# Kernel optimization log

Measured on AMD Instinct MI355X. Metric: run time of the kernel, lower is better.

## Reference

```python
import jax, jax.numpy as jnp
import numpy as np

B, T, D = 4, 2048, 2048
H = 16
HO = D // H  # head_out = 128


def setup_inputs() -> dict:
    key = jax.random.key(0)
    ks = jax.random.split(key, 6)
    x = jax.random.normal(ks[0], (B, T, D), dtype=jnp.float32)
    scale = 0.02
    Wq = jax.random.normal(ks[1], (D, D), dtype=jnp.float32) * scale
    Wk = jax.random.normal(ks[2], (D, D), dtype=jnp.float32) * scale
    Wv = jax.random.normal(ks[3], (D, D), dtype=jnp.float32) * scale
    Wp = jax.random.normal(ks[4], (D, D), dtype=jnp.float32) * scale
    bp = jnp.zeros((D,), dtype=jnp.float32)
    return {"x": x, "Wq": Wq, "Wk": Wk, "Wv": Wv, "Wp": Wp, "bp": bp}


def reference(x, Wq, Wk, Wv, Wp, bp):
    b, t, _ = x.shape
    # QKV projections (weights stored [d_in, d_out])
    q = x @ Wq
    k = x @ Wk
    v = x @ Wv
    split = lambda a: a.reshape(b, t, H, HO).transpose(0, 2, 1, 3)  # [b,H,T,ho]
    qh, kh, vh = split(q), split(k), split(v)
    # Feature attention: contract over tokens -> [b,H,ho,ho]
    scores = jnp.einsum('bhtf,bhtg->bhfg', qh, kh) / jnp.sqrt(jnp.float32(HO))
    weights = jax.nn.softmax(scores, axis=-1)  # dropout p=0.0 (identity)
    # feature_alibi: [1/T, 1/(T-1), ..., 1], broadcast over batch/head/feature
    feat_alibi = (1.0 / jnp.arange(t, 0, -1, dtype=jnp.float32)).reshape(1, 1, t, 1)
    vh = vh + feat_alibi
    # (weights @ v^T)^T : ctx[b,h,t,f] = sum_g weights[b,h,f,g] * v[b,h,t,g]
    ctx = jnp.einsum('bhfg,bhtg->bhtf', weights, vh)
    ctx = ctx.transpose(0, 2, 1, 3).reshape(b, t, H * HO)  # [b,T,d_out]
    return ctx @ Wp + bp
```

## Files before the change

### kernel.cpp

```cpp
#include <hip/hip_runtime.h>
#include <hip/hip_bf16.h>


#define Tt 2048
#define Dd 2048
#define Mm 8192

typedef __attribute__((ext_vector_type(4))) float f32x4;
typedef __attribute__((ext_vector_type(8))) short s16x8;
static_assert(sizeof(s16x8) == 16, "frag size");

typedef const __attribute__((address_space(1))) void* gptr_t;
typedef __attribute__((address_space(3))) void* lptr_t;

__device__ __forceinline__ float bf2f(ushort u) {
    union { unsigned int i; float f; } c; c.i = ((unsigned int)u) << 16; return c.f;
}
__device__ __forceinline__ ushort f2bf(float f) {
    union { float f; unsigned int i; } c; c.f = f;
    return (ushort)((c.i + 0x7FFFu + ((c.i >> 16) & 1u)) >> 16);
}
__device__ __forceinline__ void gload16(const void* g, void* l) {
    __builtin_amdgcn_global_load_lds((gptr_t)g, (lptr_t)l, 16, 0, 0);
}
__device__ __forceinline__ s16x8 ldfrag(const char* p) { return *(const s16x8*)p; }

#define MFMA_BF16(d, a, b) \
    d = __builtin_amdgcn_mfma_f32_16x16x32_bf16((a), (b), (d), 0, 0, 0)


__global__ __launch_bounds__(256) void convxT_kernel(const float* __restrict__ x,
        ushort* __restrict__ xb, ushort* __restrict__ xT) {
    __shared__ float tile[64][65];
    const int b = blockIdx.z;
    const int t0 = blockIdx.y * 64, d0 = blockIdx.x * 64;
    const int r4 = threadIdx.x >> 6, c = threadIdx.x & 63;
#pragma unroll
    for (int i = 0; i < 16; i++) {
        const int row = i * 4 + r4;
        const size_t g = ((size_t)b * Tt + t0 + row) * Dd + d0 + c;
        const float val = x[g];
        xb[g] = f2bf(val);
        tile[row][c] = val;
    }
    __syncthreads();
#pragma unroll
    for (int i = 0; i < 16; i++) {
        const int row = i * 4 + r4;
        xT[(size_t)b * ((size_t)Dd * Tt) + (size_t)(d0 + row) * Tt + t0 + c] =
            f2bf(tile[c][row]);
    }
}

__global__ __launch_bounds__(256) void transw_kernel(const float* __restrict__ W0,
        const float* __restrict__ W1, const float* __restrict__ W2,
        const float* __restrict__ W3, ushort* __restrict__ Wt) {
    __shared__ float tile[64][65];
    const int z = blockIdx.z;
    const float* W = (z == 0) ? W0 : (z == 1) ? W1 : (z == 2) ? W2 : W3;
    ushort* dst = Wt + (size_t)z * ((size_t)Dd * Dd);
    const int n0 = blockIdx.x * 64, k0 = blockIdx.y * 64;
    const int r4 = threadIdx.x >> 6, c = threadIdx.x & 63;
#pragma unroll
    for (int i = 0; i < 16; i++) {
        const int row = i * 4 + r4;
        tile[row][c] = W[(size_t)(k0 + row) * Dd + n0 + c];
    }
    __syncthreads();
#pragma unroll
    for (int i = 0; i < 16; i++) {
        const int row = i * 4 + r4;
        dst[(size_t)(n0 + row) * Dd + k0 + c] = f2bf(tile[c][row]);
    }
}


__device__ __forceinline__ void stage_half(char* ldsRegion, const ushort* gRegion,
                                           int ld, int half, int tid) {
#pragma unroll
    for (int j = 0; j < 2; j++) {
        const int Pb = half * 16384 + j * 8192 + (tid >> 6) * 1024;
        const int P = Pb + (tid & 63) * 16;
        const int row = P >> 7;
        const int colb = (P ^ ((row & 7) << 4)) & 127;
        gload16(gRegion + (size_t)row * ld + (colb >> 1), ldsRegion + Pb);
    }
}

template <int MODE>
__global__ __launch_bounds__(512, 2) void gemm256_kernel(
        const ushort* __restrict__ A, const ushort* __restrict__ Bt,
        void* __restrict__ Cv, const float* __restrict__ bias,
        int Kdim, int lda, int ldb, int ldc,
        size_t astride, size_t bstride, size_t cstride) {
    extern __shared__ char lds[];

    const int tid = threadIdx.x;
    const int lane = tid & 63;
    const int w = tid >> 6;
    const int wr = w >> 2, wc = w & 3;
    const int fr = lane & 15, fq = lane >> 4;

    const int bid = blockIdx.x;
    const int cpx = (int)gridDim.x >> 3;
    const int wg = (bid & 7) * cpx + (bid >> 3);
    const int m0 = (wg >> 3) * 256;
    const int n0 = (wg & 7) * 256;

    const ushort* Ag = A + (size_t)blockIdx.z * astride + (size_t)m0 * lda;
    const ushort* Bg = Bt + (size_t)blockIdx.z * bstride + (size_t)n0 * ldb;
    const int NT = Kdim >> 6;

    const int aoff = wr * 16384 + fr * 128;
    const int boff = wc * 8192 + fr * 128;
    const int xo = (fr & 7) << 4;
    const int cp0 = (fq * 16) ^ xo;
    const int cp1 = (64 + fq * 16) ^ xo;

    char* buf0 = lds;
    char* buf1 = lds + 65536;
    const char* Ab0 = buf0 + aoff;
    const char* Bb0 = buf0 + 32768 + boff;
    const char* Ab1 = buf1 + aoff;
    const char* Bb1 = buf1 + 32768 + boff;

    f32x4 acc[8][4];
#pragma unroll
    for (int i = 0; i < 8; i++)
#pragma unroll
        for (int j = 0; j < 4; j++) acc[i][j] = {0.f, 0.f, 0.f, 0.f};

    s16x8 afX[4][2], afY[4][2], bf01[2][2], bf23[2][2];

    {
        stage_half(buf0,         Ag, lda, 0, tid);
        stage_half(buf0,         Ag, lda, 1, tid);
        stage_half(buf0 + 32768, Bg, ldb, 0, tid);
        stage_half(buf0 + 32768, Bg, ldb, 1, tid);
        stage_half(buf1,         Ag + 64, lda, 0, tid);
        stage_half(buf1,         Ag + 64, lda, 1, tid);
        stage_half(buf1 + 32768, Bg + 64, ldb, 0, tid);
        stage_half(buf1 + 32768, Bg + 64, ldb, 1, tid);
        __builtin_amdgcn_sched_barrier(0);
        asm volatile("s_waitcnt vmcnt(8)" ::: "memory");
        __builtin_amdgcn_s_barrier();
    }

    const int NI = NT >> 1;
    for (int j = 0; j < NI; ++j) {
        const int e = 2 * j;
        const bool sAo = (j > 0);
        const bool sE2 = (e + 2 < NT);
        const bool sO2 = (e + 3 < NT);
        const ushort* AgO  = Ag + (size_t)(e + 1) * 64;
        const ushort* AgE2 = Ag + (size_t)(e + 2) * 64;
        const ushort* BgE2 = Bg + (size_t)(e + 2) * 64;
        const ushort* BgO2 = Bg + (size_t)(e + 3) * 64;

#pragma unroll
        for (int m = 0; m < 4; m++) {
            afX[m][0] = ldfrag(Ab0 + m * 2048 + cp0);
            afX[m][1] = ldfrag(Ab0 + m * 2048 + cp1);
        }
#pragma unroll
        for (int n = 0; n < 2; n++) {
            bf01[n][0] = ldfrag(Bb0 + n * 2048 + cp0);
            bf01[n][1] = ldfrag(Bb0 + n * 2048 + cp1);
        }
        if (sAo) stage_half(buf1, AgO, lda, 0, tid);
        __builtin_amdgcn_sched_barrier(0);
        asm volatile("s_waitcnt lgkmcnt(8)" ::: "memory");
        __builtin_amdgcn_s_barrier();
        asm volatile("s_waitcnt lgkmcnt(0)" ::: "memory");
        __builtin_amdgcn_sched_barrier(0);
        __builtin_amdgcn_s_setprio(1);
#pragma unroll
        for (int k = 0; k < 2; k++)
#pragma unroll
            for (int m = 0; m < 4; m++)
#pragma unroll
                for (int n = 0; n < 2; n++) MFMA_BF16(acc[m][n], afX[m][k], bf01[n][k]);
        __builtin_amdgcn_s_setprio(0);
        __builtin_amdgcn_s_barrier();

#pragma unroll
        for (int n = 0; n < 2; n++) {
            bf23[n][0] = ldfrag(Bb0 + (n + 2) * 2048 + cp0);
            bf23[n][1] = ldfrag(Bb0 + (n + 2) * 2048 + cp1);
        }
        if (sAo) stage_half(buf1, AgO, lda, 1, tid);
        __builtin_amdgcn_sched_barrier(0);
        __builtin_amdgcn_s_barrier();
        asm volatile("s_waitcnt lgkmcnt(0)" ::: "memory");
        __builtin_amdgcn_sched_barrier(0);
        __builtin_amdgcn_s_setprio(1);
#pragma unroll
        for (int k = 0; k < 2; k++)
#pragma unroll
            for (int m = 0; m < 4; m++)
#pragma unroll
                for (int n = 0; n < 2; n++) MFMA_BF16(acc[m][n + 2], afX[m][k], bf23[n][k]);
        __builtin_amdgcn_s_setprio(0);
        __builtin_amdgcn_s_barrier();

#pragma unroll
        for (int m = 0; m < 4; m++) {
            afY[m][0] = ldfrag(Ab0 + (m + 4) * 2048 + cp0);
            afY[m][1] = ldfrag(Ab0 + (m + 4) * 2048 + cp1);
        }
        if (sE2) stage_half(buf0 + 32768, BgE2, ldb, 0, tid);
        __builtin_amdgcn_sched_barrier(0);
        __builtin_amdgcn_s_barrier();
        asm volatile("s_waitcnt lgkmcnt(0)" ::: "memory");
        __builtin_amdgcn_sched_barrier(0);
        __builtin_amdgcn_s_setprio(1);
#pragma unroll
        for (int k = 0; k < 2; k++)
#pragma unroll
            for (int m = 0; m < 4; m++)
#pragma unroll
                for (int n = 0; n < 2; n++) MFMA_BF16(acc[m + 4][n], afY[m][k], bf01[n][k]);
        __builtin_amdgcn_s_setprio(0);
        __builtin_amdgcn_s_barrier();

        if (sE2) stage_half(buf0 + 32768, BgE2, ldb, 1, tid);
        __builtin_amdgcn_sched_barrier(0);
        __builtin_amdgcn_s_setprio(1);
#pragma unroll
        for (int k = 0; k < 2; k++)
#pragma unroll
            for (int m = 0; m < 4; m++)
#pragma unroll
                for (int n = 0; n < 2; n++) MFMA_BF16(acc[m + 4][n + 2], afY[m][k], bf23[n][k]);
        __builtin_amdgcn_s_setprio(0);
        __builtin_amdgcn_sched_barrier(0);
        if (sE2) asm volatile("s_waitcnt vmcnt(4)" ::: "memory");
        else     asm volatile("s_waitcnt vmcnt(0)" ::: "memory");
        __builtin_amdgcn_s_barrier();

#pragma unroll
        for (int m = 0; m < 4; m++) {
            afX[m][0] = ldfrag(Ab1 + m * 2048 + cp0);
            afX[m][1] = ldfrag(Ab1 + m * 2048 + cp1);
        }
#pragma unroll
        for (int n = 0; n < 2; n++) {
            bf01[n][0] = ldfrag(Bb1 + n * 2048 + cp0);
            bf01[n][1] = ldfrag(Bb1 + n * 2048 + cp1);
        }
        if (sE2) stage_half(buf0, AgE2, lda, 0, tid);
        __builtin_amdgcn_sched_barrier(0);
        asm volatile("s_waitcnt lgkmcnt(8)" ::: "memory");
        __builtin_amdgcn_s_barrier();
        asm volatile("s_waitcnt lgkmcnt(0)" ::: "memory");
        __builtin_amdgcn_sched_barrier(0);
        __builtin_amdgcn_s_setprio(1);
#pragma unroll
        for (int k = 0; k < 2; k++)
#pragma unroll
            for (int m = 0; m < 4; m++)
#pragma unroll
                for (int n = 0; n < 2; n++) MFMA_BF16(acc[m][n], afX[m][k], bf01[n][k]);
        __builtin_amdgcn_s_setprio(0);
        __builtin_amdgcn_s_barrier();

#pragma unroll
        for (int n = 0; n < 2; n++) {
            bf23[n][0] = ldfrag(Bb1 + (n + 2) * 2048 + cp0);
            bf23[n][1] = ldfrag(Bb1 + (n + 2) * 2048 + cp1);
        }
        if (sE2) stage_half(buf0, AgE2, lda, 1, tid);
        __builtin_amdgcn_sched_barrier(0);
        __builtin_amdgcn_s_barrier();
        asm volatile("s_waitcnt lgkmcnt(0)" ::: "memory");
        __builtin_amdgcn_sched_barrier(0);
        __builtin_amdgcn_s_setprio(1);
#pragma unroll
        for (int k = 0; k < 2; k++)
#pragma unroll
            for (int m = 0; m < 4; m++)
#pragma unroll
                for (int n = 0; n < 2; n++) MFMA_BF16(acc[m][n + 2], afX[m][k], bf23[n][k]);
        __builtin_amdgcn_s_setprio(0);
        __builtin_amdgcn_s_barrier();

#pragma unroll
        for (int m = 0; m < 4; m++) {
            afY[m][0] = ldfrag(Ab1 + (m + 4) * 2048 + cp0);
            afY[m][1] = ldfrag(Ab1 + (m + 4) * 2048 + cp1);
        }
        if (sO2) stage_half(buf1 + 32768, BgO2, ldb, 0, tid);
        __builtin_amdgcn_sched_barrier(0);
        __builtin_amdgcn_s_barrier();
        asm volatile("s_waitcnt lgkmcnt(0)" ::: "memory");
        __builtin_amdgcn_sched_barrier(0);
        __builtin_amdgcn_s_setprio(1);
#pragma unroll
        for (int k = 0; k < 2; k++)
#pragma unroll
            for (int m = 0; m < 4; m++)
#pragma unroll
                for (int n = 0; n < 2; n++) MFMA_BF16(acc[m + 4][n], afY[m][k], bf01[n][k]);
        __builtin_amdgcn_s_setprio(0);
        __builtin_amdgcn_s_barrier();

        if (sO2) stage_half(buf1 + 32768, BgO2, ldb, 1, tid);
        __builtin_amdgcn_sched_barrier(0);
        __builtin_amdgcn_s_setprio(1);
#pragma unroll
        for (int k = 0; k < 2; k++)
#pragma unroll
            for (int m = 0; m < 4; m++)
#pragma unroll
                for (int n = 0; n < 2; n++) MFMA_BF16(acc[m + 4][n + 2], afY[m][k], bf23[n][k]);
        __builtin_amdgcn_s_setprio(0);
        __builtin_amdgcn_sched_barrier(0);
        if (sO2) asm volatile("s_waitcnt vmcnt(4)" ::: "memory");
        else     asm volatile("s_waitcnt vmcnt(0)" ::: "memory");
        __builtin_amdgcn_s_barrier();
    }

    if (MODE == 2) {
        float* C = (float*)Cv;
#pragma unroll
        for (int mi = 0; mi < 8; mi++)
#pragma unroll
            for (int ni = 0; ni < 4; ni++)
#pragma unroll
                for (int r = 0; r < 4; r++) {
                    const int row = m0 + wr * 128 + mi * 16 + fq * 4 + r;
                    const int col = n0 + wc * 64 + ni * 16 + fr;
                    C[(size_t)row * ldc + col] = acc[mi][ni][r] + bias[col];
                }
    } else {
        ushort* C = (ushort*)Cv + (size_t)blockIdx.z * cstride;
#pragma unroll
        for (int mi = 0; mi < 8; mi++)
#pragma unroll
            for (int ni = 0; ni < 4; ni++)
#pragma unroll
                for (int r = 0; r < 4; r++) {
                    const int row = m0 + wr * 128 + mi * 16 + fq * 4 + r;
                    const int col = n0 + wc * 64 + ni * 16 + fr;
                    C[(size_t)row * ldc + col] = f2bf(acc[mi][ni][r]);
                }
    }
}


template <int MODE>
__global__ __launch_bounds__(256, 2) void gemm_kernel(
        const ushort* __restrict__ A, const ushort* __restrict__ Bt,
        void* __restrict__ Cv, const float* __restrict__ bias,
        int Kdim, int lda, int ldb, int ldc) {
    __shared__ ushort lsA[128 * 32];
    __shared__ ushort lsB[128 * 32];

    const int tid = threadIdx.x;
    const int w = tid >> 6, lane = tid & 63;
    const int m0 = blockIdx.y * 128;
    const int n0 = blockIdx.x * 128;

    const ushort* Ab = A;
    const ushort* Bb = Bt;
    size_t coff = 0;
    if (MODE == 1) {
        const int z = blockIdx.z, b = z >> 4, h = z & 15;
        const size_t ao = (size_t)b * ((size_t)Tt * Dd) + (size_t)h * 128;
        Ab += ao; Bb += (size_t)z * (128 * 128); coff = ao;
    }
    if (MODE == 3) {
        const int z = blockIdx.z, s = z >> 6, bh = z & 63;
        const int b = bh >> 4, h = bh & 15;
        Ab += (size_t)h * 128 * Dd + (size_t)s * 512;
        Bb += (size_t)b * ((size_t)Dd * Dd) + (size_t)h * 128 * Dd + (size_t)s * 512;
        coff = (size_t)s * (64 * 16384) + (size_t)bh * 16384;
    }

    const int sr = lane >> 2;
    const int sc = (lane & 3) * 8;
    const int c0 = w, c1 = w + 4;
    const int rA0 = c0 * 16 + sr, rA1 = c1 * 16 + sr;

    const int fr = lane & 15, fq = lane >> 4;
    const int wr = (w >> 1) * 64, wc = (w & 1) * 64;

    f32x4 acc[4][4];
#pragma unroll
    for (int i = 0; i < 4; i++)
#pragma unroll
        for (int j = 0; j < 4; j++) acc[i][j] = {0.f, 0.f, 0.f, 0.f};

    for (int kt = 0; kt < Kdim; kt += 32) {
        gload16(Ab + (size_t)(m0 + rA0) * lda + kt + sc, lsA + c0 * 512);
        gload16(Ab + (size_t)(m0 + rA1) * lda + kt + sc, lsA + c1 * 512);
        gload16(Bb + (size_t)(n0 + rA0) * ldb + kt + sc, lsB + c0 * 512);
        gload16(Bb + (size_t)(n0 + rA1) * ldb + kt + sc, lsB + c1 * 512);
        __syncthreads();

        s16x8 afrag[4], bfrag[4];
#pragma unroll
        for (int i = 0; i < 4; i++)
            afrag[i] = *(const s16x8*)(lsA + (wr + i * 16 + fr) * 32 + fq * 8);
#pragma unroll
        for (int j = 0; j < 4; j++)
            bfrag[j] = *(const s16x8*)(lsB + (wc + j * 16 + fr) * 32 + fq * 8);
#pragma unroll
        for (int i = 0; i < 4; i++)
#pragma unroll
            for (int j = 0; j < 4; j++)
                MFMA_BF16(acc[i][j], afrag[i], bfrag[j]);
        __syncthreads();
    }

    if (MODE == 3) {
        float* C = (float*)Cv + coff;
#pragma unroll
        for (int i = 0; i < 4; i++)
#pragma unroll
            for (int j = 0; j < 4; j++)
#pragma unroll
                for (int r = 0; r < 4; r++) {
                    const int row = m0 + wr + i * 16 + fq * 4 + r;
                    const int col = n0 + wc + j * 16 + fr;
                    C[(size_t)row * ldc + col] = acc[i][j][r];
                }
    } else {
        ushort* C = (ushort*)Cv + coff;
#pragma unroll
        for (int i = 0; i < 4; i++)
#pragma unroll
            for (int j = 0; j < 4; j++)
#pragma unroll
                for (int r = 0; r < 4; r++) {
                    const int row = m0 + wr + i * 16 + fq * 4 + r;
                    const int col = n0 + wc + j * 16 + fr;
                    float val = acc[i][j][r];
                    if (MODE == 1) val += 1.0f / (float)(Tt - row);
                    C[(size_t)row * ldc + col] = f2bf(val);
                }
    }
}


__global__ __launch_bounds__(256) void softmax_kernel(const float* __restrict__ part,
                                                      ushort* __restrict__ wts) {
    const int tid = threadIdx.x;
    const int wv = tid >> 6, lane = tid & 63;
    const int row = blockIdx.x * 4 + wv;
    const float* p = part + (size_t)row * 128 + lane * 2;
    float v0 = 0.f, v1 = 0.f;
#pragma unroll
    for (int s = 0; s < 4; s++) {
        const float2 t = *(const float2*)(p + (size_t)s * 1048576);
        v0 += t.x; v1 += t.y;
    }
    const float sc = 0.088388347648318447f;
    v0 *= sc; v1 *= sc;
    float m = fmaxf(v0, v1);
#pragma unroll
    for (int off = 32; off > 0; off >>= 1) m = fmaxf(m, __shfl_xor(m, off));
    const float e0 = __expf(v0 - m), e1 = __expf(v1 - m);
    float smv = e0 + e1;
#pragma unroll
    for (int off = 32; off > 0; off >>= 1) smv += __shfl_xor(smv, off);
    const float inv = 1.0f / smv;
    ushort2 o; o.x = f2bf(e0 * inv); o.y = f2bf(e1 * inv);
    *(ushort2*)(wts + (size_t)row * 128 + lane * 2) = o;
}


extern "C" void kernel_launch(void* const* d_in, const int* in_sizes, int n_in,
                              void* d_out, int out_size, void* d_ws, size_t ws_size,
                              hipStream_t stream) {
    const float* x  = (const float*)d_in[0];
    const float* Wq = (const float*)d_in[1];
    const float* Wk = (const float*)d_in[2];
    const float* Wv = (const float*)d_in[3];
    const float* Wp = (const float*)d_in[4];
    const float* bp = (const float*)d_in[5];
    float* out = (float*)d_out;
    char* ws = (char*)d_ws;

    ushort* xb  = (ushort*)(ws);
    ushort* xT  = (ushort*)(ws + (32ull << 20));
    ushort* Wt  = (ushort*)(ws + (64ull << 20));
    ushort* G   = (ushort*)(ws + (96ull << 20));
    ushort* Hb  = (ushort*)(ws + (128ull << 20));
    ushort* v   = (ushort*)(ws + (160ull << 20));
    float*  part = (float*)(ws + (96ull << 20));
    ushort* wts = (ushort*)(ws + (112ull << 20));
    ushort* ctx = xT;

    const size_t WSZ = (size_t)Dd * Dd;

    static_cast<void>(hipFuncSetAttribute((const void*)gemm256_kernel<0>,
        hipFuncAttributeMaxDynamicSharedMemorySize, 131072));
    static_cast<void>(hipFuncSetAttribute((const void*)gemm256_kernel<2>,
        hipFuncAttributeMaxDynamicSharedMemorySize, 131072));

    convxT_kernel<<<dim3(32, 32, 4), 256, 0, stream>>>(x, xb, xT);
    transw_kernel<<<dim3(32, 32, 4), 256, 0, stream>>>(Wq, Wk, Wv, Wp, Wt);

    gemm256_kernel<0><<<dim3(64, 1, 4), 512, 131072, stream>>>(
        xT, xT, G, nullptr, 2048, 2048, 2048, 2048, WSZ, WSZ, WSZ);

    gemm256_kernel<0><<<dim3(64, 1, 4), 512, 131072, stream>>>(
        Wt + WSZ, G, Hb, nullptr, 2048, 2048, 2048, 2048, 0, WSZ, WSZ);

    gemm256_kernel<0><<<dim3(256, 1, 1), 512, 131072, stream>>>(
        xb, Wt + 2 * WSZ, v, nullptr, 2048, 2048, 2048, 2048, 0, 0, 0);

    gemm_kernel<3><<<dim3(1, 1, 256), 256, 0, stream>>>(
        Wt, Hb, part, nullptr, 512, 2048, 2048, 128);

    softmax_kernel<<<2048, 256, 0, stream>>>(part, wts);

    gemm_kernel<1><<<dim3(1, 16, 64), 256, 0, stream>>>(
        v, wts, ctx, nullptr, 128, 2048, 128, 2048);

    gemm256_kernel<2><<<dim3(256, 1, 1), 512, 131072, stream>>>(
        ctx, Wt + 3 * WSZ, out, bp, 2048, 2048, 2048, 2048, 0, 0, 0);
}
```

Before: 337.3 us.

## Fold softmax weights into the output projection and apply alibi via Wp column sums

The weights are no longer applied to v to build ctx. Each batch now gets a combined matrix M_b, with the per-head softmax weights folded into Wp. The final GEMM becomes a batched v @ M_b whose epilogue adds alibi[t]*colsum(Wp) plus the bias. The column sums are accumulated with atomics in the weight-transpose kernel, and softmax writes transposed weights for the new fold. Total GEMM work stays about the same, so this mainly reshapes data flow. In exchange it adds a memset, atomics and a batched final GEMM with per-batch B operands, which gets less L2 reuse.

```diff
diff --git a/kernel.cpp b/kernel.cpp
--- a/kernel.cpp
+++ b/kernel.cpp
@@ -52,9 +52,11 @@
     }
 }
 
+
 __global__ __launch_bounds__(256) void transw_kernel(const float* __restrict__ W0,
         const float* __restrict__ W1, const float* __restrict__ W2,
-        const float* __restrict__ W3, ushort* __restrict__ Wt) {
+        const float* __restrict__ W3, ushort* __restrict__ Wt,
+        float* __restrict__ S) {
     __shared__ float tile[64][65];
     const int z = blockIdx.z;
     const float* W = (z == 0) ? W0 : (z == 1) ? W1 : (z == 2) ? W2 : W3;
@@ -72,6 +74,12 @@
         const int row = i * 4 + r4;
         dst[(size_t)(n0 + row) * Dd + k0 + c] = f2bf(tile[c][row]);
     }
+    if (z == 3) {
+        float partial = 0.f;
+#pragma unroll
+        for (int i = 0; i < 16; i++) partial += tile[r4 * 16 + i][c];
+        atomicAdd(&S[n0 + c], partial);
+    }
 }
 
 
@@ -91,6 +99,7 @@
 __global__ __launch_bounds__(512, 2) void gemm256_kernel(
         const ushort* __restrict__ A, const ushort* __restrict__ Bt,
         void* __restrict__ Cv, const float* __restrict__ bias,
+        const float* __restrict__ S,
         int Kdim, int lda, int ldb, int ldc,
         size_t astride, size_t bstride, size_t cstride) {
     extern __shared__ char lds[];
@@ -321,7 +330,7 @@
     }
 
     if (MODE == 2) {
-        float* C = (float*)Cv;
+        float* C = (float*)Cv + (size_t)blockIdx.z * cstride;
 #pragma unroll
         for (int mi = 0; mi < 8; mi++)
 #pragma unroll
@@ -330,7 +339,9 @@
                 for (int r = 0; r < 4; r++) {
                     const int row = m0 + wr * 128 + mi * 16 + fq * 4 + r;
                     const int col = n0 + wc * 64 + ni * 16 + fr;
-                    C[(size_t)row * ldc + col] = acc[mi][ni][r] + bias[col];
+                    const float alibi = 1.0f / (float)(Tt - row);
+                    C[(size_t)row * ldc + col] =
+                        acc[mi][ni][r] + alibi * S[col] + bias[col];
                 }
     } else {
         ushort* C = (ushort*)Cv + (size_t)blockIdx.z * cstride;
@@ -351,7 +362,7 @@
 template <int MODE>
 __global__ __launch_bounds__(256, 2) void gemm_kernel(
         const ushort* __restrict__ A, const ushort* __restrict__ Bt,
-        void* __restrict__ Cv, const float* __restrict__ bias,
+        void* __restrict__ Cv,
         int Kdim, int lda, int ldb, int ldc) {
     __shared__ ushort lsA[128 * 32];
     __shared__ ushort lsB[128 * 32];
@@ -364,17 +375,18 @@
     const ushort* Ab = A;
     const ushort* Bb = Bt;
     size_t coff = 0;
-    if (MODE == 1) {
-        const int z = blockIdx.z, b = z >> 4, h = z & 15;
-        const size_t ao = (size_t)b * ((size_t)Tt * Dd) + (size_t)h * 128;
-        Ab += ao; Bb += (size_t)z * (128 * 128); coff = ao;
-    }
     if (MODE == 3) {
         const int z = blockIdx.z, s = z >> 6, bh = z & 63;
         const int b = bh >> 4, h = bh & 15;
         Ab += (size_t)h * 128 * Dd + (size_t)s * 512;
         Bb += (size_t)b * ((size_t)Dd * Dd) + (size_t)h * 128 * Dd + (size_t)s * 512;
         coff = (size_t)s * (64 * 16384) + (size_t)bh * 16384;
+    }
+    if (MODE == 4) {
+        const int z = blockIdx.z, b = z >> 4, h = z & 15;
+        Ab += (size_t)h * 128;
+        Bb += (size_t)z * 16384;
+        coff = (size_t)b * ((size_t)Dd * Dd) + (size_t)h * 128;
     }
 
     const int sr = lane >> 2;
@@ -435,16 +447,14 @@
                 for (int r = 0; r < 4; r++) {
                     const int row = m0 + wr + i * 16 + fq * 4 + r;
                     const int col = n0 + wc + j * 16 + fr;
-                    float val = acc[i][j][r];
-                    if (MODE == 1) val += 1.0f / (float)(Tt - row);
-                    C[(size_t)row * ldc + col] = f2bf(val);
+                    C[(size_t)row * ldc + col] = f2bf(acc[i][j][r]);
                 }
     }
 }
 
 
 __global__ __launch_bounds__(256) void softmax_kernel(const float* __restrict__ part,
-                                                      ushort* __restrict__ wts) {
+                                                      ushort* __restrict__ wtsT) {
     const int tid = threadIdx.x;
     const int wv = tid >> 6, lane = tid & 63;
     const int row = blockIdx.x * 4 + wv;
@@ -465,8 +475,10 @@
 #pragma unroll
     for (int off = 32; off > 0; off >>= 1) smv += __shfl_xor(smv, off);
     const float inv = 1.0f / smv;
-    ushort2 o; o.x = f2bf(e0 * inv); o.y = f2bf(e1 * inv);
-    *(ushort2*)(wts + (size_t)row * 128 + lane * 2) = o;
+    const int bh = row >> 7, f = row & 127;
+    ushort* o = wtsT + (size_t)bh * 16384 + (size_t)(lane * 2) * 128 + f;
+    o[0]   = f2bf(e0 * inv);
+    o[128] = f2bf(e1 * inv);
 }
 
 
@@ -482,43 +494,46 @@
     float* out = (float*)d_out;
     char* ws = (char*)d_ws;
 
-    ushort* xb  = (ushort*)(ws);
-    ushort* xT  = (ushort*)(ws + (32ull << 20));
-    ushort* Wt  = (ushort*)(ws + (64ull << 20));
-    ushort* G   = (ushort*)(ws + (96ull << 20));
-    ushort* Hb  = (ushort*)(ws + (128ull << 20));
-    ushort* v   = (ushort*)(ws + (160ull << 20));
-    float*  part = (float*)(ws + (96ull << 20));
-    ushort* wts = (ushort*)(ws + (112ull << 20));
-    ushort* ctx = xT;
+    ushort* xb   = (ushort*)(ws);
+    ushort* xT   = (ushort*)(ws + (32ull << 20));
+    ushort* Wt   = (ushort*)(ws + (64ull << 20));
+    ushort* G    = (ushort*)(ws + (96ull << 20));
+    ushort* Hb   = (ushort*)(ws + (128ull << 20));
+    ushort* v    = (ushort*)(ws + (160ull << 20));
+    float*  part = (float*) (ws + (96ull << 20));
+    ushort* wtsT = (ushort*)(ws + (112ull << 20));
+    float*  S    = (float*) (ws + (194ull << 20));
+    ushort* Mt   = xT;
 
     const size_t WSZ = (size_t)Dd * Dd;
+    const size_t TD  = (size_t)Tt * Dd;
 
     static_cast<void>(hipFuncSetAttribute((const void*)gemm256_kernel<0>,
         hipFuncAttributeMaxDynamicSharedMemorySize, 131072));
     static_cast<void>(hipFuncSetAttribute((const void*)gemm256_kernel<2>,
         hipFuncAttributeMaxDynamicSharedMemorySize, 131072));
 
+    static_cast<void>(hipMemsetAsync(S, 0, Dd * sizeof(float), stream));
     convxT_kernel<<<dim3(32, 32, 4), 256, 0, stream>>>(x, xb, xT);
-    transw_kernel<<<dim3(32, 32, 4), 256, 0, stream>>>(Wq, Wk, Wv, Wp, Wt);
+    transw_kernel<<<dim3(32, 32, 4), 256, 0, stream>>>(Wq, Wk, Wv, Wp, Wt, S);
 
     gemm256_kernel<0><<<dim3(64, 1, 4), 512, 131072, stream>>>(
-        xT, xT, G, nullptr, 2048, 2048, 2048, 2048, WSZ, WSZ, WSZ);
+        xT, xT, G, nullptr, nullptr, 2048, 2048, 2048, 2048, WSZ, WSZ, WSZ);
 
     gemm256_kernel<0><<<dim3(64, 1, 4), 512, 131072, stream>>>(
-        Wt + WSZ, G, Hb, nullptr, 2048, 2048, 2048, 2048, 0, WSZ, WSZ);
+        Wt + WSZ, G, Hb, nullptr, nullptr, 2048, 2048, 2048, 2048, 0, WSZ, WSZ);
 
     gemm256_kernel<0><<<dim3(256, 1, 1), 512, 131072, stream>>>(
-        xb, Wt + 2 * WSZ, v, nullptr, 2048, 2048, 2048, 2048, 0, 0, 0);
+        xb, Wt + 2 * WSZ, v, nullptr, nullptr, 2048, 2048, 2048, 2048, 0, 0, 0);
 
     gemm_kernel<3><<<dim3(1, 1, 256), 256, 0, stream>>>(
-        Wt, Hb, part, nullptr, 512, 2048, 2048, 128);
-
-    softmax_kernel<<<2048, 256, 0, stream>>>(part, wts);
-
-    gemm_kernel<1><<<dim3(1, 16, 64), 256, 0, stream>>>(
-        v, wts, ctx, nullptr, 128, 2048, 128, 2048);
-
-    gemm256_kernel<2><<<dim3(256, 1, 1), 512, 131072, stream>>>(
-        ctx, Wt + 3 * WSZ, out, bp, 2048, 2048, 2048, 2048, 0, 0, 0);
-}
+        Wt, Hb, part, 512, 2048, 2048, 128);
+
+    softmax_kernel<<<2048, 256, 0, stream>>>(part, wtsT);
+
+    gemm_kernel<4><<<dim3(1, 16, 64), 256, 0, stream>>>(
+        Wt + 3 * WSZ, wtsT, Mt, 128, 2048, 128, 2048);
+
+    gemm256_kernel<2><<<dim3(64, 1, 4), 512, 131072, stream>>>(
+        v, Mt, out, bp, S, 2048, 2048, 2048, 2048, TD, WSZ, TD);
+}
```

After: 353.2 us. 1.05x slower.
